# Optimization experiments

Measured on AMD Instinct MI355X. Metric: run time of the kernel, lower is better.

The kernel has to match this reference:

```python
import jax, jax.numpy as jnp
import numpy as np

N, E, H = 100000, 640000, 64
DIN_N, DIN_E, L, OUT = 32, 16, 2, 1
BN_EPS = 1e-5


def setup_inputs() -> dict:
    key = jax.random.key(0)
    ks = iter(jax.random.split(key, 40))
    def p(shape, s=0.05):
        return jax.random.normal(next(ks), shape, dtype=jnp.float32) * s
    return {
        "x": jax.random.normal(next(ks), (N, DIN_N), dtype=jnp.float32),
        "edge_attr": jax.random.normal(next(ks), (E, DIN_E), dtype=jnp.float32),
        "src": jax.random.randint(next(ks), (E,), 0, N),
        "dst": jax.random.randint(next(ks), (E,), 0, N),
        "node_emb_w": p((DIN_N, H)), "node_emb_b": p((H,)),
        "edge_emb_w": p((DIN_E, H)), "edge_emb_b": p((H,)),
        "lin_edge_w": p((L, H, H)), "lin_edge_b": p((L, H)),
        "conv_w1": p((L, H, H)), "conv_b1": p((L, H)),
        "conv_w2": p((L, H, H)), "conv_b2": p((L, H)),
        "emlp_w1": p((L, 3 * H, H)), "emlp_b1": p((L, H)),
        "emlp_w2": p((L, H, H)), "emlp_b2": p((L, H)),
        "bn_gamma": jnp.ones((L, H), jnp.float32),
        "bn_beta": jnp.zeros((L, H), jnp.float32),
        "mlp_w1": p((3 * H, 50)), "mlp_b1": p((50,)),
        "mlp_w2": p((50, 25)), "mlp_b2": p((25,)),
        "mlp_w3": p((25, OUT)), "mlp_b3": p((OUT,)),
    }


def _batchnorm(h, gamma, beta):
    # training-mode BatchNorm1d over the node axis (biased variance)
    mu = jnp.mean(h, axis=0)
    var = jnp.mean(jnp.square(h - mu), axis=0)
    return gamma * (h - mu) * jax.lax.rsqrt(var + BN_EPS) + beta


def _forward(x, edge_attr, src, dst,
             node_emb_w, node_emb_b, edge_emb_w, edge_emb_b,
             lin_edge_w, lin_edge_b, conv_w1, conv_b1, conv_w2, conv_b2,
             emlp_w1, emlp_b1, emlp_w2, emlp_b2, bn_gamma, bn_beta,
             mlp_w1, mlp_b1, mlp_w2, mlp_b2, mlp_w3, mlp_b3):
    x = x @ node_emb_w + node_emb_b                       # [N, H]
    e = edge_attr @ edge_emb_w + edge_emb_b               # [E, H]
    for i in range(L):
        # GINEConv (eps=0): msg = ReLU(x_src + Lin(edge_attr)); sum at dst
        msg = jax.nn.relu(x[src] + e @ lin_edge_w[i] + lin_edge_b[i])
        agg = jax.ops.segment_sum(msg, dst, num_segments=N)
        h = x + agg
        h = jax.nn.relu(h @ conv_w1[i] + conv_b1[i]) @ conv_w2[i] + conv_b2[i]
        x = (x + jax.nn.relu(_batchnorm(h, bn_gamma[i], bn_beta[i]))) / 2
        cat = jnp.concatenate([x[src], x[dst], e], axis=-1)  # [E, 3H]
        upd = jax.nn.relu(cat @ emlp_w1[i] + emlp_b1[i]) @ emlp_w2[i] + emlp_b2[i]
        e = e + upd / 2
    # edge readout: relu(cat(x_src, x_dst)) ++ edge_attr -> MLP (dropout off/eval)
    er = jnp.concatenate(
        [jax.nn.relu(jnp.concatenate([x[src], x[dst]], axis=-1)), e], axis=-1)
    hmid = jax.nn.relu(er @ mlp_w1 + mlp_b1)
    hmid = jax.nn.relu(hmid @ mlp_w2 + mlp_b2)
    logit = hmid @ mlp_w3 + mlp_b3
    return x, logit


def reference(x, edge_attr, src, dst,
              node_emb_w, node_emb_b, edge_emb_w, edge_emb_b,
              lin_edge_w, lin_edge_b, conv_w1, conv_b1, conv_w2, conv_b2,
              emlp_w1, emlp_b1, emlp_w2, emlp_b2, bn_gamma, bn_beta,
              mlp_w1, mlp_b1, mlp_w2, mlp_b2, mlp_w3, mlp_b3):
    return _forward(x, edge_attr, src, dst,
                    node_emb_w, node_emb_b, edge_emb_w, edge_emb_b,
                    lin_edge_w, lin_edge_b, conv_w1, conv_b1, conv_w2, conv_b2,
                    emlp_w1, emlp_b1, emlp_w2, emlp_b2, bn_gamma, bn_beta,
                    mlp_w1, mlp_b1, mlp_w2, mlp_b2, mlp_w3, mlp_b3)
```

## Files before the change

### kernel.cpp

```cpp
#include <hip/hip_runtime.h>

#define NN 100000
#define NE 640000
#define NB_SCAN 98

typedef __attribute__((ext_vector_type(8))) short short8;
typedef __attribute__((ext_vector_type(4))) float f32x4;
typedef __attribute__((ext_vector_type(4))) ushort ushort4v;

__device__ __forceinline__ float bf2f(ushort u) {
    unsigned v = ((unsigned)u) << 16;
    return __builtin_bit_cast(float, v);
}
__device__ __forceinline__ ushort f2bf(float f) {
    unsigned u = __builtin_bit_cast(unsigned, f);
    u += 0x7fffu + ((u >> 16) & 1u);
    return (ushort)(u >> 16);
}
__device__ __forceinline__ short8 brelu(short8 v) {
    #pragma unroll
    for (int i = 0; i < 8; ++i) v[i] = (v[i] < (short)0) ? (short)0 : v[i];
    return v;
}

__global__ void k_hist(const int* __restrict__ dst, int* __restrict__ hist)
{
    int i = blockIdx.x * 256 + threadIdx.x;
    atomicAdd(&hist[dst[i]], 1);
}

__global__ __launch_bounds__(256) void k_scan_part(const int* __restrict__ hist,
                                                   int* __restrict__ rp,
                                                   int* __restrict__ parts)
{
    __shared__ int s[256];
    int b = blockIdx.x, t = threadIdx.x;
    int base = b * 1024 + t * 4;
    int v[4]; int sum = 0;
    #pragma unroll
    for (int i = 0; i < 4; ++i) { int idx = base + i; v[i] = (idx < NN) ? hist[idx] : 0; sum += v[i]; }
    s[t] = sum; __syncthreads();
    for (int off = 1; off < 256; off <<= 1) {
        int x = (t >= off) ? s[t - off] : 0;
        __syncthreads(); s[t] += x; __syncthreads();
    }
    int excl = s[t] - sum;
    if (t == 255) parts[b] = s[255];
    int run = excl;
    #pragma unroll
    for (int i = 0; i < 4; ++i) { int idx = base + i; if (idx < NN) rp[idx] = run; run += v[i]; }
}

__global__ void k_scan_tops(int* __restrict__ parts, int* __restrict__ rp)
{
    __shared__ int s[128];
    int t = threadIdx.x;
    int v = (t < NB_SCAN) ? parts[t] : 0;
    s[t] = v; __syncthreads();
    for (int off = 1; off < 128; off <<= 1) {
        int x = (t >= off) ? s[t - off] : 0;
        __syncthreads(); s[t] += x; __syncthreads();
    }
    parts[t] = s[t] - v;
    if (t == 0) rp[NN] = NE;
}

__global__ __launch_bounds__(256) void k_scan_add(int* __restrict__ rp,
                                                  const int* __restrict__ parts,
                                                  int* __restrict__ cursor)
{
    int i = blockIdx.x * 256 + threadIdx.x;
    if (i >= NN) return;
    int v = rp[i] + parts[i >> 10];
    rp[i] = v; cursor[i] = v;
}

__global__ void k_scatter(const int* __restrict__ dst,
                          int* __restrict__ cursor, int* __restrict__ spos)
{
    int i = blockIdx.x * 256 + threadIdx.x;
    int d = dst[i];
    int p = atomicAdd(&cursor[d], 1);
    spos[i] = p;
}

__global__ void k_w_subtile(const float* __restrict__ w, ushort* __restrict__ out,
                            int K, int Nin)
{
    int t = blockIdx.x * 256 + threadIdx.x;
    if (t >= K * 64) return;
    int k = t >> 6, c = t & 63;
    float v = (c < Nin) ? w[k * Nin + c] : 0.f;
    out[((k >> 3) * 64 + c) * 8 + (k & 7)] = f2bf(v);
}

__global__ void k_w_padk(const float* __restrict__ w, ushort* __restrict__ out,
                         int Kreal, int Kpad)
{
    int t = blockIdx.x * 256 + threadIdx.x;
    if (t >= Kpad * 64) return;
    int k = t >> 6, c = t & 63;
    float v = (k < Kreal) ? w[k * 64 + c] : 0.f;
    out[((k >> 3) * 64 + c) * 8 + (k & 7)] = f2bf(v);
}

__global__ void k_w_msg(const float* __restrict__ lw, ushort* __restrict__ out)
{
    int t = blockIdx.x * 256 + threadIdx.x;
    if (t >= 128 * 64) return;
    int k = t >> 6, c = t & 63;
    float v = (k < 64) ? (k == c ? 1.f : 0.f) : lw[(k - 64) * 64 + c];
    out[((k >> 3) * 64 + c) * 8 + (k & 7)] = f2bf(v);
}

__global__ __launch_bounds__(256) void k_node_emb_mfma(
    const float* __restrict__ xin, const ushort* __restrict__ ws,
    const float* __restrict__ b, float* __restrict__ xout,
    ushort* __restrict__ xb)
{
    __shared__ ushort wl[32 * 64];
    __shared__ float fbuf[4][16 * 64];
    __shared__ ushort bbuf[4][16 * 64];
    int tid = threadIdx.x;
    *(short8*)&wl[tid * 8] = *(const short8*)&ws[tid * 8];
    __syncthreads();

    int wid = tid >> 6, lane = tid & 63, c = lane & 15, kg = lane >> 4;
    int t = blockIdx.x * 4 + wid;
    if (t >= NN / 16) return;
    int n0 = t * 16;

    const float* xr = xin + (size_t)(n0 + c) * 32 + kg * 8;
    f32x4 u0 = *(const f32x4*)xr, u1 = *(const f32x4*)(xr + 4);
    short8 a;
    #pragma unroll
    for (int j = 0; j < 4; ++j) { a[j] = (short)f2bf(u0[j]); a[4 + j] = (short)f2bf(u1[j]); }

    f32x4 acc[4];
    #pragma unroll
    for (int nt = 0; nt < 4; ++nt) {
        float bv = b[nt * 16 + c];
        acc[nt] = f32x4{bv, bv, bv, bv};
        short8 bf = *(const short8*)&wl[(kg * 64 + nt * 16 + c) * 8];
        acc[nt] = __builtin_amdgcn_mfma_f32_16x16x32_bf16(a, bf, acc[nt], 0, 0, 0);
    }
    #pragma unroll
    for (int nt = 0; nt < 4; ++nt)
        #pragma unroll
        for (int i = 0; i < 4; ++i) {
            int rr = kg * 4 + i, cc = nt * 16 + c;
            float v = acc[nt][i];
            fbuf[wid][rr * 64 + cc] = v;
            bbuf[wid][rr * 64 + cc] = f2bf(v);
        }
    #pragma unroll
    for (int r = 0; r < 4; ++r) {
        int q = r * 64 + lane;
        *(f32x4*)&xout[(size_t)(n0 + (q >> 4)) * 64 + (q & 15) * 4] =
            *(f32x4*)&fbuf[wid][q * 4];
    }
    #pragma unroll
    for (int r = 0; r < 2; ++r) {
        int q = r * 64 + lane;
        *(short8*)&xb[(size_t)(n0 + (q >> 3)) * 64 + (q & 7) * 8] =
            *(short8*)&bbuf[wid][q * 8];
    }
}

__global__ __launch_bounds__(256) void k_edge_emb_fused(
    const float* __restrict__ ein, const ushort* __restrict__ ws,
    const float* __restrict__ b, ushort* __restrict__ eb,
    const ushort* __restrict__ xb, const int* __restrict__ src,
    const int* __restrict__ spos, const ushort* __restrict__ wm,
    const float* __restrict__ lb, ushort* __restrict__ msgbuf)
{
    __shared__ ushort wl[32 * 64];
    __shared__ ushort wml[128 * 64];
    __shared__ ushort bbuf[4][16 * 72];
    int tid = threadIdx.x;
    *(short8*)&wl[tid * 8] = *(const short8*)&ws[tid * 8];
    #pragma unroll
    for (int i = 0; i < 4; ++i)
        *(short8*)&wml[(i * 256 + tid) * 8] = *(const short8*)&wm[(i * 256 + tid) * 8];
    __syncthreads();

    int wid = tid >> 6, lane = tid & 63, c = lane & 15, kg = lane >> 4;
    int e0 = (blockIdx.x * 4 + wid) * 16;
    ushort* bb = bbuf[wid];

    short8 a = (short8)0;
    if (kg < 2) {
        const float* er = ein + (size_t)(e0 + c) * 16 + kg * 8;
        f32x4 u0 = *(const f32x4*)er, u1 = *(const f32x4*)(er + 4);
        #pragma unroll
        for (int j = 0; j < 4; ++j) { a[j] = (short)f2bf(u0[j]); a[4 + j] = (short)f2bf(u1[j]); }
    }
    f32x4 acc[4];
    #pragma unroll
    for (int nt = 0; nt < 4; ++nt) {
        float bv = b[nt * 16 + c];
        acc[nt] = f32x4{bv, bv, bv, bv};
        short8 bf = *(const short8*)&wl[(kg * 64 + nt * 16 + c) * 8];
        acc[nt] = __builtin_amdgcn_mfma_f32_16x16x32_bf16(a, bf, acc[nt], 0, 0, 0);
    }
    #pragma unroll
    for (int nt = 0; nt < 4; ++nt)
        #pragma unroll
        for (int i = 0; i < 4; ++i)
            bb[(kg * 4 + i) * 72 + nt * 16 + c] = f2bf(acc[nt][i]);
    #pragma unroll
    for (int r = 0; r < 2; ++r) {
        int q = r * 64 + lane;
        *(short8*)&eb[(size_t)(e0 + (q >> 3)) * 64 + (q & 7) * 8] =
            *(short8*)&bb[(q >> 3) * 72 + (q & 7) * 8];
    }
    short8 en0 = *(const short8*)&bb[c * 72 + kg * 8];
    short8 en1 = *(const short8*)&bb[c * 72 + 32 + kg * 8];
    const ushort* xs = xb + (size_t)src[e0 + c] * 64;
    short8 a0 = *(const short8*)(xs + kg * 8);
    short8 a1 = *(const short8*)(xs + 32 + kg * 8);

    f32x4 acc3[4];
    #pragma unroll
    for (int nt = 0; nt < 4; ++nt) {
        float bv = lb[nt * 16 + c];
        acc3[nt] = f32x4{bv, bv, bv, bv};
    }
    short8 af[4] = {a0, a1, en0, en1};
    #pragma unroll
    for (int ks = 0; ks < 4; ++ks) {
        #pragma unroll
        for (int nt = 0; nt < 4; ++nt) {
            short8 bf = *(const short8*)&wml[((ks * 4 + kg) * 64 + nt * 16 + c) * 8];
            acc3[nt] = __builtin_amdgcn_mfma_f32_16x16x32_bf16(af[ks], bf, acc3[nt], 0, 0, 0);
        }
    }
    #pragma unroll
    for (int nt = 0; nt < 4; ++nt)
        #pragma unroll
        for (int i = 0; i < 4; ++i)
            bb[(kg * 4 + i) * 72 + nt * 16 + c] = f2bf(fmaxf(acc3[nt][i], 0.f));
    int p = spos[e0 + c];
    *(short8*)&msgbuf[(size_t)p * 64 + kg * 8]      = *(short8*)&bb[c * 72 + kg * 8];
    *(short8*)&msgbuf[(size_t)p * 64 + 32 + kg * 8] = *(short8*)&bb[c * 72 + 32 + kg * 8];
}

__global__ __launch_bounds__(256) void k_conv_csr(
    const float* __restrict__ x, const ushort* __restrict__ msgbuf,
    const int* __restrict__ rp, float* __restrict__ hout,
    const ushort* __restrict__ w1s, const float* __restrict__ b1,
    const ushort* __restrict__ w2s, const float* __restrict__ b2,
    float* __restrict__ stats)
{
    __shared__ ushort w1l[64 * 64];
    __shared__ ushort w2l[64 * 64];
    __shared__ ushort h1l[4][1024];
    __shared__ float red[2][4][64];
    int tid = threadIdx.x;
    #pragma unroll
    for (int i = 0; i < 2; ++i) {
        *(short8*)&w1l[(i * 256 + tid) * 8] = *(const short8*)&w1s[(i * 256 + tid) * 8];
        *(short8*)&w2l[(i * 256 + tid) * 8] = *(const short8*)&w2s[(i * 256 + tid) * 8];
    }
    __syncthreads();

    int wid = tid >> 6, lane = tid & 63;
    int c = lane & 15, kg = lane >> 4;

    short8 w2f[2][4];
    #pragma unroll
    for (int ks = 0; ks < 2; ++ks)
        #pragma unroll
        for (int nt = 0; nt < 4; ++nt)
            w2f[ks][nt] = *(const short8*)&w2l[((ks * 4 + kg) * 64 + nt * 16 + c) * 8];

    float b1v[4], b2v[4];
    #pragma unroll
    for (int nt = 0; nt < 4; ++nt) { b1v[nt] = b1[nt * 16 + c]; b2v[nt] = b2[nt * 16 + c]; }

    float s1[4] = {0.f, 0.f, 0.f, 0.f}, s2[4] = {0.f, 0.f, 0.f, 0.f};
    ushort* hl = h1l[wid];

    int t = blockIdx.x * 4 + wid;
    if (t < NN / 16) {
        int n0 = t * 16;
        int n = n0 + c;
        int jb = rp[n], je = rp[n + 1];
        float sm0[8] = {0,0,0,0,0,0,0,0}, sm1[8] = {0,0,0,0,0,0,0,0};
        for (int j = jb; j < je; ++j) {
            short8 m0 = *(const short8*)&msgbuf[(size_t)j * 64 + kg * 8];
            short8 m1 = *(const short8*)&msgbuf[(size_t)j * 64 + 32 + kg * 8];
            #pragma unroll
            for (int i = 0; i < 8; ++i) {
                sm0[i] += bf2f((ushort)m0[i]);
                sm1[i] += bf2f((ushort)m1[i]);
            }
        }
        const float* xr = x + (size_t)n * 64;
        f32x4 u0 = *(const f32x4*)(xr + kg * 8);
        f32x4 u1 = *(const f32x4*)(xr + kg * 8 + 4);
        f32x4 v0 = *(const f32x4*)(xr + 32 + kg * 8);
        f32x4 v1 = *(const f32x4*)(xr + 32 + kg * 8 + 4);
        short8 a[2];
        #pragma unroll
        for (int j = 0; j < 4; ++j) {
            a[0][j]     = (short)f2bf(u0[j] + sm0[j]);
            a[0][4 + j] = (short)f2bf(u1[j] + sm0[4 + j]);
            a[1][j]     = (short)f2bf(v0[j] + sm1[j]);
            a[1][4 + j] = (short)f2bf(v1[j] + sm1[4 + j]);
        }
        f32x4 acc[4];
        #pragma unroll
        for (int nt = 0; nt < 4; ++nt) acc[nt] = f32x4{b1v[nt], b1v[nt], b1v[nt], b1v[nt]};
        #pragma unroll
        for (int ks = 0; ks < 2; ++ks) {
            #pragma unroll
            for (int nt = 0; nt < 4; ++nt) {
                short8 bf = *(const short8*)&w1l[((ks * 4 + kg) * 64 + nt * 16 + c) * 8];
                acc[nt] = __builtin_amdgcn_mfma_f32_16x16x32_bf16(a[ks], bf, acc[nt], 0, 0, 0);
            }
        }
        #pragma unroll
        for (int nt = 0; nt < 4; ++nt) {
            #pragma unroll
            for (int i = 0; i < 4; ++i) {
                int rr = kg * 4 + i, cc = nt * 16 + c;
                hl[((cc >> 3) * 16 + rr) * 8 + (cc & 7)] = f2bf(fmaxf(acc[nt][i], 0.f));
            }
        }
        f32x4 acc2[4];
        #pragma unroll
        for (int nt = 0; nt < 4; ++nt) acc2[nt] = f32x4{b2v[nt], b2v[nt], b2v[nt], b2v[nt]};
        #pragma unroll
        for (int ks = 0; ks < 2; ++ks) {
            short8 ha = *(const short8*)&hl[((ks * 4 + kg) * 16 + c) * 8];
            #pragma unroll
            for (int nt = 0; nt < 4; ++nt)
                acc2[nt] = __builtin_amdgcn_mfma_f32_16x16x32_bf16(ha, w2f[ks][nt], acc2[nt], 0, 0, 0);
        }
        #pragma unroll
        for (int nt = 0; nt < 4; ++nt) {
            #pragma unroll
            for (int i = 0; i < 4; ++i) {
                int rr = kg * 4 + i, cc = nt * 16 + c;
                float h2 = acc2[nt][i];
                hout[(size_t)(n0 + rr) * 64 + cc] = h2;
                s1[nt] += h2;
                s2[nt] += h2 * h2;
            }
        }
    }
    #pragma unroll
    for (int nt = 0; nt < 4; ++nt) {
        float v1 = s1[nt], v2 = s2[nt];
        v1 += __shfl_xor(v1, 16); v1 += __shfl_xor(v1, 32);
        v2 += __shfl_xor(v2, 16); v2 += __shfl_xor(v2, 32);
        s1[nt] = v1; s2[nt] = v2;
    }
    if (lane < 16) {
        #pragma unroll
        for (int nt = 0; nt < 4; ++nt) {
            red[0][wid][nt * 16 + c] = s1[nt];
            red[1][wid][nt * 16 + c] = s2[nt];
        }
    }
    __syncthreads();
    if (wid == 0) {
        float a = red[0][0][lane] + red[0][1][lane] + red[0][2][lane] + red[0][3][lane];
        float b = red[1][0][lane] + red[1][1][lane] + red[1][2][lane] + red[1][3][lane];
        unsafeAtomicAdd(&stats[lane], a);
        unsafeAtomicAdd(&stats[64 + lane], b);
    }
}

__global__ void k_bnfin(float* __restrict__ stats,
                        const float* __restrict__ gamma,
                        const float* __restrict__ beta)
{
    int j = threadIdx.x;
    float mu = stats[j] * (1.f / NN);
    float var = stats[64 + j] * (1.f / NN) - mu * mu;
    float a = gamma[j] * rsqrtf(var + 1e-5f);
    stats[128 + j] = a;
    stats[192 + j] = beta[j] - mu * a;
}

__global__ __launch_bounds__(256) void k_xupd4(float* __restrict__ x,
                                               const float* __restrict__ h,
                                               const float* __restrict__ stats,
                                               ushort* __restrict__ xb)
{
    int idx = blockIdx.x * 256 + threadIdx.x;
    int j4 = (idx & 15) * 4;
    f32x4 hv = *(const f32x4*)&h[(size_t)idx * 4];
    f32x4 xv = *(const f32x4*)&x[(size_t)idx * 4];
    f32x4 av = *(const f32x4*)&stats[128 + j4];
    f32x4 cv = *(const f32x4*)&stats[192 + j4];
    f32x4 xo;
    ushort4v bo;
    #pragma unroll
    for (int i = 0; i < 4; ++i) {
        float r = fmaxf(fmaf(hv[i], av[i], cv[i]), 0.f);
        float xn = (xv[i] + r) * 0.5f;
        xo[i] = xn;
        bo[i] = f2bf(xn);
    }
    *(f32x4*)&x[(size_t)idx * 4] = xo;
    *(ushort4v*)&xb[(size_t)idx * 4] = bo;
}

template<int NEXT>
__global__ __launch_bounds__(512) void k_emlp_fused(
    const ushort* __restrict__ xb, ushort* __restrict__ eb,
    const int* __restrict__ src, const int* __restrict__ dst,
    const ushort* __restrict__ w1s, const float* __restrict__ b1,
    const ushort* __restrict__ w2s, const float* __restrict__ b2,
    const ushort* __restrict__ wm, const float* __restrict__ lbn,
    const int* __restrict__ spos, ushort* __restrict__ msgbuf)
{
    __shared__ ushort w1l[192 * 64];
    __shared__ ushort w2l[64 * 64];
    __shared__ ushort wml[NEXT ? 128 * 64 : 8];
    __shared__ ushort hb[8][1152];
    int tid = threadIdx.x;
    #pragma unroll
    for (int i = 0; i < 3; ++i)
        *(short8*)&w1l[(i * 512 + tid) * 8] = *(const short8*)&w1s[(i * 512 + tid) * 8];
    *(short8*)&w2l[tid * 8] = *(const short8*)&w2s[tid * 8];
    if (NEXT) {
        #pragma unroll
        for (int i = 0; i < 2; ++i)
            *(short8*)&wml[(i * 512 + tid) * 8] = *(const short8*)&wm[(i * 512 + tid) * 8];
    }
    __syncthreads();

    int wid = tid >> 6, lane = tid & 63;
    int c = lane & 15, kg = lane >> 4;

    float b1v[4], b2v[4], lbv[4];
    #pragma unroll
    for (int nt = 0; nt < 4; ++nt) {
        b1v[nt] = b1[nt * 16 + c];
        b2v[nt] = b2[nt * 16 + c];
        lbv[nt] = NEXT ? lbn[nt * 16 + c] : 0.f;
    }
    ushort* hl = hb[wid];

    #pragma unroll 1
    for (int t4 = 0; t4 < 4; ++t4) {
        int e0 = blockIdx.x * 512 + wid * 64 + t4 * 16;
        int myedge = e0 + c;
        int s = src[myedge], d = dst[myedge];
        const ushort* xs = xb + (size_t)s * 64;
        const ushort* xd = xb + (size_t)d * 64;
        const ushort* ee = eb + (size_t)myedge * 64;
        short8 a[6];
        a[0] = *(const short8*)(xs + kg * 8);
        a[1] = *(const short8*)(xs + 32 + kg * 8);
        a[2] = *(const short8*)(xd + kg * 8);
        a[3] = *(const short8*)(xd + 32 + kg * 8);
        a[4] = *(const short8*)(ee + kg * 8);
        a[5] = *(const short8*)(ee + 32 + kg * 8);

        f32x4 acc[4];
        #pragma unroll
        for (int nt = 0; nt < 4; ++nt) acc[nt] = f32x4{b1v[nt], b1v[nt], b1v[nt], b1v[nt]};
        #pragma unroll
        for (int ks = 0; ks < 6; ++ks) {
            #pragma unroll
            for (int nt = 0; nt < 4; ++nt) {
                short8 bf = *(const short8*)&w1l[((ks * 4 + kg) * 64 + nt * 16 + c) * 8];
                acc[nt] = __builtin_amdgcn_mfma_f32_16x16x32_bf16(a[ks], bf, acc[nt], 0, 0, 0);
            }
        }
        #pragma unroll
        for (int nt = 0; nt < 4; ++nt) {
            #pragma unroll
            for (int i = 0; i < 4; ++i) {
                int rr = kg * 4 + i, cc = nt * 16 + c;
                hl[((cc >> 3) * 16 + rr) * 8 + (cc & 7)] = f2bf(fmaxf(acc[nt][i], 0.f));
            }
        }
        f32x4 acc2[4];
        #pragma unroll
        for (int nt = 0; nt < 4; ++nt) acc2[nt] = f32x4{b2v[nt], b2v[nt], b2v[nt], b2v[nt]};
        #pragma unroll
        for (int ks = 0; ks < 2; ++ks) {
            short8 ha = *(const short8*)&hl[((ks * 4 + kg) * 16 + c) * 8];
            #pragma unroll
            for (int nt = 0; nt < 4; ++nt) {
                short8 bf = *(const short8*)&w2l[((ks * 4 + kg) * 64 + nt * 16 + c) * 8];
                acc2[nt] = __builtin_amdgcn_mfma_f32_16x16x32_bf16(ha, bf, acc2[nt], 0, 0, 0);
            }
        }
        #pragma unroll
        for (int nt = 0; nt < 4; ++nt)
            #pragma unroll
            for (int i = 0; i < 4; ++i)
                hl[(kg * 4 + i) * 72 + nt * 16 + c] = f2bf(acc2[nt][i]);
        short8 u0 = *(const short8*)&hl[c * 72 + kg * 8];
        short8 u1 = *(const short8*)&hl[c * 72 + 32 + kg * 8];
        short8 en0, en1;
        #pragma unroll
        for (int j = 0; j < 8; ++j) {
            en0[j] = (short)f2bf(bf2f((ushort)a[4][j]) + 0.5f * bf2f((ushort)u0[j]));
            en1[j] = (short)f2bf(bf2f((ushort)a[5][j]) + 0.5f * bf2f((ushort)u1[j]));
        }
        *(short8*)&eb[(size_t)myedge * 64 + kg * 8]      = en0;
        *(short8*)&eb[(size_t)myedge * 64 + 32 + kg * 8] = en1;

        if (NEXT) {
            f32x4 acc3[4];
            #pragma unroll
            for (int nt = 0; nt < 4; ++nt) acc3[nt] = f32x4{lbv[nt], lbv[nt], lbv[nt], lbv[nt]};
            short8 af[4] = {a[0], a[1], en0, en1};
            #pragma unroll
            for (int ks = 0; ks < 4; ++ks) {
                #pragma unroll
                for (int nt = 0; nt < 4; ++nt) {
                    short8 bf = *(const short8*)&wml[((ks * 4 + kg) * 64 + nt * 16 + c) * 8];
                    acc3[nt] = __builtin_amdgcn_mfma_f32_16x16x32_bf16(af[ks], bf, acc3[nt], 0, 0, 0);
                }
            }
            #pragma unroll
            for (int nt = 0; nt < 4; ++nt)
                #pragma unroll
                for (int i = 0; i < 4; ++i)
                    hl[(kg * 4 + i) * 72 + nt * 16 + c] = f2bf(fmaxf(acc3[nt][i], 0.f));
            int p = spos[myedge];
            *(short8*)&msgbuf[(size_t)p * 64 + kg * 8]      = *(short8*)&hl[c * 72 + kg * 8];
            *(short8*)&msgbuf[(size_t)p * 64 + 32 + kg * 8] = *(short8*)&hl[c * 72 + 32 + kg * 8];
        }
    }
}

__global__ __launch_bounds__(256) void k_readout_mfma(
    const ushort* __restrict__ xb, const ushort* __restrict__ eb,
    const int* __restrict__ src, const int* __restrict__ dst,
    const ushort* __restrict__ w1s, const float* __restrict__ b1,
    const float* __restrict__ w2, const float* __restrict__ b2,
    const float* __restrict__ w3, const float* __restrict__ b3,
    float* __restrict__ logit)
{
    __shared__ ushort w1l[192 * 64];
    __shared__ ushort hw[4][64 * 50];
    int tid = threadIdx.x;
    #pragma unroll
    for (int i = 0; i < 6; ++i)
        *(short8*)&w1l[(i * 256 + tid) * 8] = *(const short8*)&w1s[(i * 256 + tid) * 8];
    __syncthreads();

    int wid = tid >> 6, lane = tid & 63;
    int c = lane & 15, kg = lane >> 4;
    float b1v[4];
    #pragma unroll
    for (int nt = 0; nt < 4; ++nt) b1v[nt] = (nt * 16 + c < 50) ? b1[nt * 16 + c] : 0.f;

    #pragma unroll 1
    for (int t4 = 0; t4 < 4; ++t4) {
        int e0 = blockIdx.x * 256 + wid * 64 + t4 * 16;
        int myedge = e0 + c;
        int s = src[myedge], d = dst[myedge];
        const ushort* xs = xb + (size_t)s * 64;
        const ushort* xd = xb + (size_t)d * 64;
        const ushort* ee = eb + (size_t)myedge * 64;
        short8 a[6];
        a[0] = brelu(*(const short8*)(xs + kg * 8));
        a[1] = brelu(*(const short8*)(xs + 32 + kg * 8));
        a[2] = brelu(*(const short8*)(xd + kg * 8));
        a[3] = brelu(*(const short8*)(xd + 32 + kg * 8));
        a[4] = *(const short8*)(ee + kg * 8);
        a[5] = *(const short8*)(ee + 32 + kg * 8);

        f32x4 acc[4];
        #pragma unroll
        for (int nt = 0; nt < 4; ++nt) acc[nt] = f32x4{b1v[nt], b1v[nt], b1v[nt], b1v[nt]};
        #pragma unroll
        for (int ks = 0; ks < 6; ++ks) {
            #pragma unroll
            for (int nt = 0; nt < 4; ++nt) {
                short8 bf = *(const short8*)&w1l[((ks * 4 + kg) * 64 + nt * 16 + c) * 8];
                acc[nt] = __builtin_amdgcn_mfma_f32_16x16x32_bf16(a[ks], bf, acc[nt], 0, 0, 0);
            }
        }
        #pragma unroll
        for (int nt = 0; nt < 4; ++nt) {
            #pragma unroll
            for (int i = 0; i < 4; ++i) {
                int rr = kg * 4 + i, cc = nt * 16 + c;
                if (cc < 50)
                    hw[wid][(t4 * 16 + rr) * 50 + cc] = f2bf(fmaxf(acc[nt][i], 0.f));
            }
        }
    }
    int edge = blockIdx.x * 256 + wid * 64 + lane;
    const ushort* hrow = &hw[wid][lane * 50];
    float a25[25];
    #pragma unroll
    for (int j = 0; j < 25; ++j) a25[j] = b2[j];
    #pragma unroll 2
    for (int k = 0; k < 50; ++k) {
        float hv = bf2f(hrow[k]);
        #pragma unroll
        for (int j = 0; j < 25; ++j) a25[j] = fmaf(hv, w2[k * 25 + j], a25[j]);
    }
    float lg = b3[0];
    #pragma unroll
    for (int k = 0; k < 25; ++k) lg = fmaf(fmaxf(a25[k], 0.f), w3[k], lg);
    logit[edge] = lg;
}

extern "C" void kernel_launch(void* const* d_in, const int* in_sizes, int n_in,
                              void* d_out, int out_size, void* d_ws, size_t ws_size,
                              hipStream_t stream)
{
    const float* x_in  = (const float*)d_in[0];
    const float* eattr = (const float*)d_in[1];
    const int*   src   = (const int*)d_in[2];
    const int*   dst   = (const int*)d_in[3];
    const float* n_w   = (const float*)d_in[4];
    const float* n_b   = (const float*)d_in[5];
    const float* e_w   = (const float*)d_in[6];
    const float* e_b   = (const float*)d_in[7];
    const float* lw    = (const float*)d_in[8];
    const float* lb    = (const float*)d_in[9];
    const float* cw1   = (const float*)d_in[10];
    const float* cb1   = (const float*)d_in[11];
    const float* cw2   = (const float*)d_in[12];
    const float* cb2   = (const float*)d_in[13];
    const float* ew1   = (const float*)d_in[14];
    const float* eb1   = (const float*)d_in[15];
    const float* ew2   = (const float*)d_in[16];
    const float* eb2   = (const float*)d_in[17];
    const float* gam   = (const float*)d_in[18];
    const float* bet   = (const float*)d_in[19];
    const float* m1w   = (const float*)d_in[20];
    const float* m1b   = (const float*)d_in[21];
    const float* m2w   = (const float*)d_in[22];
    const float* m2b   = (const float*)d_in[23];
    const float* m3w   = (const float*)d_in[24];
    const float* m3b   = (const float*)d_in[25];

    float* xbuf  = (float*)d_out;
    float* logit = xbuf + (size_t)NN * 64;

    ushort* eb     = (ushort*)d_ws;
    float*  tmp    = (float*)(eb + (size_t)NE * 64);
    float*  stats  = tmp + (size_t)NN * 64;
    ushort* w1s    = (ushort*)(stats + 256);
    ushort* w2s    = w1s + 2 * 192 * 64;
    ushort* m1s    = w2s + 2 * 64 * 64;
    ushort* xb     = m1s + 192 * 64;
    ushort* wms    = xb + (size_t)NN * 64;
    ushort* cw1s   = wms + 2 * 128 * 64;
    ushort* cw2s   = cw1s + 2 * 64 * 64;
    ushort* nws    = cw2s + 2 * 64 * 64;
    ushort* ews    = nws + 32 * 64;
    ushort* msgbuf = ews + 32 * 64;
    int*    hist   = (int*)(msgbuf + (size_t)NE * 64);
    int*    rp     = hist + NN;
    int*    cursor = rp + NN + 1;
    int*    parts  = cursor + NN;
    int*    spos   = parts + 128;

    hipMemsetAsync(hist, 0, NN * sizeof(int), stream);
    k_hist<<<NE / 256, 256, 0, stream>>>(dst, hist);
    k_scan_part<<<NB_SCAN, 256, 0, stream>>>(hist, rp, parts);
    k_scan_tops<<<1, 128, 0, stream>>>(parts, rp);
    k_scan_add<<<(NN + 255) / 256, 256, 0, stream>>>(rp, parts, cursor);
    k_scatter<<<NE / 256, 256, 0, stream>>>(dst, cursor, spos);

    k_w_subtile<<<48, 256, 0, stream>>>(ew1,            w1s,            192, 64);
    k_w_subtile<<<48, 256, 0, stream>>>(ew1 + 192 * 64, w1s + 192 * 64, 192, 64);
    k_w_subtile<<<16, 256, 0, stream>>>(ew2,            w2s,            64, 64);
    k_w_subtile<<<16, 256, 0, stream>>>(ew2 + 64 * 64,  w2s + 64 * 64,  64, 64);
    k_w_subtile<<<48, 256, 0, stream>>>(m1w,            m1s,            192, 50);
    k_w_msg<<<32, 256, 0, stream>>>(lw,           wms);
    k_w_msg<<<32, 256, 0, stream>>>(lw + 64 * 64, wms + 128 * 64);
    k_w_subtile<<<16, 256, 0, stream>>>(cw1,            cw1s,           64, 64);
    k_w_subtile<<<16, 256, 0, stream>>>(cw1 + 64 * 64,  cw1s + 64 * 64, 64, 64);
    k_w_subtile<<<16, 256, 0, stream>>>(cw2,            cw2s,           64, 64);
    k_w_subtile<<<16, 256, 0, stream>>>(cw2 + 64 * 64,  cw2s + 64 * 64, 64, 64);
    k_w_padk<<<8, 256, 0, stream>>>(n_w, nws, 32, 32);
    k_w_padk<<<8, 256, 0, stream>>>(e_w, ews, 16, 32);

    k_node_emb_mfma<<<(NN / 16 + 3) / 4, 256, 0, stream>>>(x_in, nws, n_b, xbuf, xb);
    k_edge_emb_fused<<<NE / 64, 256, 0, stream>>>(eattr, ews, e_b, eb,
                                                  xb, src, spos, wms, lb, msgbuf);

    for (int l = 0; l < 2; ++l) {
        hipMemsetAsync(stats, 0, 256 * sizeof(float), stream);
        k_conv_csr<<<(NN / 16 + 3) / 4, 256, 0, stream>>>(
            xbuf, msgbuf, rp, tmp, cw1s + l * 64 * 64, cb1 + l * 64,
            cw2s + l * 64 * 64, cb2 + l * 64, stats);
        k_bnfin<<<1, 64, 0, stream>>>(stats, gam + l * 64, bet + l * 64);
        k_xupd4<<<NN * 16 / 256, 256, 0, stream>>>(xbuf, tmp, stats, xb);
        if (l == 0) {
            k_emlp_fused<1><<<NE / 512, 512, 0, stream>>>(
                xb, eb, src, dst, w1s, eb1, w2s, eb2,
                wms + 128 * 64, lb + 64, spos, msgbuf);
        } else {
            k_emlp_fused<0><<<NE / 512, 512, 0, stream>>>(
                xb, eb, src, dst, w1s + 192 * 64, eb1 + 64, w2s + 64 * 64, eb2 + 64,
                wms, lb, spos, msgbuf);
        }
    }

    k_readout_mfma<<<NE / 256, 256, 0, stream>>>(xb, eb, src, dst,
                                                 m1s, m1b, m2w, m2b, m3w, m3b, logit);
}
```

Measured before the change: 607.9 us.

## Write messages in edge order and gather via CSR edge index

Messages are now written contiguously in edge order with coalesced stores instead of being scattered to destination-sorted positions. The scatter pass records a permutation array, and the CSR aggregation reads each message through that index, so the random access moves from writes to reads. Separately, the edge MLP kernel drops to 256-thread blocks and keeps the second-layer weights in registers rather than shared memory, which frees LDS for occupancy at the cost of more registers. The aggregation loop now has an extra dependent index load per edge.

Result: faster. 571.9 us (-5.9%).

```diff
diff --git a/kernel.cpp b/kernel.cpp
--- a/kernel.cpp
+++ b/kernel.cpp
@@ -76,12 +76,12 @@
 }
 
 __global__ void k_scatter(const int* __restrict__ dst,
-                          int* __restrict__ cursor, int* __restrict__ spos)
+                          int* __restrict__ cursor, int* __restrict__ eidx)
 {
     int i = blockIdx.x * 256 + threadIdx.x;
     int d = dst[i];
     int p = atomicAdd(&cursor[d], 1);
-    spos[i] = p;
+    eidx[p] = i;
 }
 
 __global__ void k_w_subtile(const float* __restrict__ w, ushort* __restrict__ out,
@@ -171,8 +171,8 @@
     const float* __restrict__ ein, const ushort* __restrict__ ws,
     const float* __restrict__ b, ushort* __restrict__ eb,
     const ushort* __restrict__ xb, const int* __restrict__ src,
-    const int* __restrict__ spos, const ushort* __restrict__ wm,
-    const float* __restrict__ lb, ushort* __restrict__ msgbuf)
+    const ushort* __restrict__ wm, const float* __restrict__ lb,
+    ushort* __restrict__ msgbuf)
 {
     __shared__ ushort wl[32 * 64];
     __shared__ ushort wml[128 * 64];
@@ -240,14 +240,18 @@
         #pragma unroll
         for (int i = 0; i < 4; ++i)
             bb[(kg * 4 + i) * 72 + nt * 16 + c] = f2bf(fmaxf(acc3[nt][i], 0.f));
-    int p = spos[e0 + c];
-    *(short8*)&msgbuf[(size_t)p * 64 + kg * 8]      = *(short8*)&bb[c * 72 + kg * 8];
-    *(short8*)&msgbuf[(size_t)p * 64 + 32 + kg * 8] = *(short8*)&bb[c * 72 + 32 + kg * 8];
+    #pragma unroll
+    for (int r = 0; r < 2; ++r) {
+        int q = r * 64 + lane;
+        *(short8*)&msgbuf[(size_t)(e0 + (q >> 3)) * 64 + (q & 7) * 8] =
+            *(short8*)&bb[(q >> 3) * 72 + (q & 7) * 8];
+    }
 }
 
 __global__ __launch_bounds__(256) void k_conv_csr(
     const float* __restrict__ x, const ushort* __restrict__ msgbuf,
-    const int* __restrict__ rp, float* __restrict__ hout,
+    const int* __restrict__ rp, const int* __restrict__ eidx,
+    float* __restrict__ hout,
     const ushort* __restrict__ w1s, const float* __restrict__ b1,
     const ushort* __restrict__ w2s, const float* __restrict__ b2,
     float* __restrict__ stats)
@@ -288,8 +292,9 @@
         int jb = rp[n], je = rp[n + 1];
         float sm0[8] = {0,0,0,0,0,0,0,0}, sm1[8] = {0,0,0,0,0,0,0,0};
         for (int j = jb; j < je; ++j) {
-            short8 m0 = *(const short8*)&msgbuf[(size_t)j * 64 + kg * 8];
-            short8 m1 = *(const short8*)&msgbuf[(size_t)j * 64 + 32 + kg * 8];
+            int row = eidx[j];
+            short8 m0 = *(const short8*)&msgbuf[(size_t)row * 64 + kg * 8];
+            short8 m1 = *(const short8*)&msgbuf[(size_t)row * 64 + 32 + kg * 8];
             #pragma unroll
             for (int i = 0; i < 8; ++i) {
                 sm0[i] += bf2f((ushort)m0[i]);
@@ -410,32 +415,37 @@
 }
 
 template<int NEXT>
-__global__ __launch_bounds__(512) void k_emlp_fused(
+__global__ __launch_bounds__(256) void k_emlp_fused(
     const ushort* __restrict__ xb, ushort* __restrict__ eb,
     const int* __restrict__ src, const int* __restrict__ dst,
     const ushort* __restrict__ w1s, const float* __restrict__ b1,
     const ushort* __restrict__ w2s, const float* __restrict__ b2,
     const ushort* __restrict__ wm, const float* __restrict__ lbn,
-    const int* __restrict__ spos, ushort* __restrict__ msgbuf)
+    ushort* __restrict__ msgbuf)
 {
     __shared__ ushort w1l[192 * 64];
-    __shared__ ushort w2l[64 * 64];
     __shared__ ushort wml[NEXT ? 128 * 64 : 8];
-    __shared__ ushort hb[8][1152];
+    __shared__ ushort hb[4][1152];
     int tid = threadIdx.x;
     #pragma unroll
-    for (int i = 0; i < 3; ++i)
-        *(short8*)&w1l[(i * 512 + tid) * 8] = *(const short8*)&w1s[(i * 512 + tid) * 8];
-    *(short8*)&w2l[tid * 8] = *(const short8*)&w2s[tid * 8];
+    for (int i = 0; i < 6; ++i)
+        *(short8*)&w1l[(i * 256 + tid) * 8] = *(const short8*)&w1s[(i * 256 + tid) * 8];
     if (NEXT) {
         #pragma unroll
-        for (int i = 0; i < 2; ++i)
-            *(short8*)&wml[(i * 512 + tid) * 8] = *(const short8*)&wm[(i * 512 + tid) * 8];
+        for (int i = 0; i < 4; ++i)
+            *(short8*)&wml[(i * 256 + tid) * 8] = *(const short8*)&wm[(i * 256 + tid) * 8];
     }
     __syncthreads();
 
     int wid = tid >> 6, lane = tid & 63;
     int c = lane & 15, kg = lane >> 4;
+
+    short8 w2f[2][4];
+    #pragma unroll
+    for (int ks = 0; ks < 2; ++ks)
+        #pragma unroll
+        for (int nt = 0; nt < 4; ++nt)
+            w2f[ks][nt] = *(const short8*)&w2s[((ks * 4 + kg) * 64 + nt * 16 + c) * 8];
 
     float b1v[4], b2v[4], lbv[4];
     #pragma unroll
@@ -448,7 +458,7 @@
 
     #pragma unroll 1
     for (int t4 = 0; t4 < 4; ++t4) {
-        int e0 = blockIdx.x * 512 + wid * 64 + t4 * 16;
+        int e0 = blockIdx.x * 256 + wid * 64 + t4 * 16;
         int myedge = e0 + c;
         int s = src[myedge], d = dst[myedge];
         const ushort* xs = xb + (size_t)s * 64;
@@ -488,10 +498,8 @@
         for (int ks = 0; ks < 2; ++ks) {
             short8 ha = *(const short8*)&hl[((ks * 4 + kg) * 16 + c) * 8];
             #pragma unroll
-            for (int nt = 0; nt < 4; ++nt) {
-                short8 bf = *(const short8*)&w2l[((ks * 4 + kg) * 64 + nt * 16 + c) * 8];
-                acc2[nt] = __builtin_amdgcn_mfma_f32_16x16x32_bf16(ha, bf, acc2[nt], 0, 0, 0);
-            }
+            for (int nt = 0; nt < 4; ++nt)
+                acc2[nt] = __builtin_amdgcn_mfma_f32_16x16x32_bf16(ha, w2f[ks][nt], acc2[nt], 0, 0, 0);
         }
         #pragma unroll
         for (int nt = 0; nt < 4; ++nt)
@@ -527,9 +535,12 @@
                 #pragma unroll
                 for (int i = 0; i < 4; ++i)
                     hl[(kg * 4 + i) * 72 + nt * 16 + c] = f2bf(fmaxf(acc3[nt][i], 0.f));
-            int p = spos[myedge];
-            *(short8*)&msgbuf[(size_t)p * 64 + kg * 8]      = *(short8*)&hl[c * 72 + kg * 8];
-            *(short8*)&msgbuf[(size_t)p * 64 + 32 + kg * 8] = *(short8*)&hl[c * 72 + 32 + kg * 8];
+            #pragma unroll
+            for (int r = 0; r < 2; ++r) {
+                int q = r * 64 + lane;
+                *(short8*)&msgbuf[(size_t)(e0 + (q >> 3)) * 64 + (q & 7) * 8] =
+                    *(short8*)&hl[(q >> 3) * 72 + (q & 7) * 8];
+            }
         }
     }
 }
@@ -661,14 +672,14 @@
     int*    rp     = hist + NN;
     int*    cursor = rp + NN + 1;
     int*    parts  = cursor + NN;
-    int*    spos   = parts + 128;
+    int*    eidx   = parts + 128;
 
     hipMemsetAsync(hist, 0, NN * sizeof(int), stream);
     k_hist<<<NE / 256, 256, 0, stream>>>(dst, hist);
     k_scan_part<<<NB_SCAN, 256, 0, stream>>>(hist, rp, parts);
     k_scan_tops<<<1, 128, 0, stream>>>(parts, rp);
     k_scan_add<<<(NN + 255) / 256, 256, 0, stream>>>(rp, parts, cursor);
-    k_scatter<<<NE / 256, 256, 0, stream>>>(dst, cursor, spos);
+    k_scatter<<<NE / 256, 256, 0, stream>>>(dst, cursor, eidx);
 
     k_w_subtile<<<48, 256, 0, stream>>>(ew1,            w1s,            192, 64);
     k_w_subtile<<<48, 256, 0, stream>>>(ew1 + 192 * 64, w1s + 192 * 64, 192, 64);
@@ -686,23 +697,23 @@
 
     k_node_emb_mfma<<<(NN / 16 + 3) / 4, 256, 0, stream>>>(x_in, nws, n_b, xbuf, xb);
     k_edge_emb_fused<<<NE / 64, 256, 0, stream>>>(eattr, ews, e_b, eb,
-                                                  xb, src, spos, wms, lb, msgbuf);
+                                                  xb, src, wms, lb, msgbuf);
 
     for (int l = 0; l < 2; ++l) {
         hipMemsetAsync(stats, 0, 256 * sizeof(float), stream);
         k_conv_csr<<<(NN / 16 + 3) / 4, 256, 0, stream>>>(
-            xbuf, msgbuf, rp, tmp, cw1s + l * 64 * 64, cb1 + l * 64,
+            xbuf, msgbuf, rp, eidx, tmp, cw1s + l * 64 * 64, cb1 + l * 64,
             cw2s + l * 64 * 64, cb2 + l * 64, stats);
         k_bnfin<<<1, 64, 0, stream>>>(stats, gam + l * 64, bet + l * 64);
         k_xupd4<<<NN * 16 / 256, 256, 0, stream>>>(xbuf, tmp, stats, xb);
         if (l == 0) {
-            k_emlp_fused<1><<<NE / 512, 512, 0, stream>>>(
+            k_emlp_fused<1><<<NE / 256, 256, 0, stream>>>(
                 xb, eb, src, dst, w1s, eb1, w2s, eb2,
-                wms + 128 * 64, lb + 64, spos, msgbuf);
+                wms + 128 * 64, lb + 64, msgbuf);
         } else {
-            k_emlp_fused<0><<<NE / 512, 512, 0, stream>>>(
+            k_emlp_fused<0><<<NE / 256, 256, 0, stream>>>(
                 xb, eb, src, dst, w1s + 192 * 64, eb1 + 64, w2s + 64 * 64, eb2 + 64,
-                wms, lb, spos, msgbuf);
+                wms, lb, msgbuf);
         }
     }
 
```
